# Kernel tuning notes

Measured on AMD Instinct MI355X. Metric: run time of the kernel, lower is better.

The kernel has to match this reference:

```python
import jax, jax.numpy as jnp
import numpy as np

S, L, V, E, H, LBL, CH = 4096, 16, 100000, 256, 512, 64, 4


def setup_inputs() -> dict:
    key = jax.random.key(0)
    ks = jax.random.split(key, 10)
    sc = lambda k, shp, fan: (jax.random.normal(k, shp, jnp.float32) / np.sqrt(fan)).astype(jnp.float32)
    return {
        "sentence": jax.random.randint(ks[0], (S,), 0, V, dtype=jnp.int32),
        "chars": jax.random.normal(ks[1], (S, L), dtype=jnp.float32),
        "char_lens": jax.random.randint(ks[2], (S,), 1, L + 1, dtype=jnp.int32),
        "emb": jax.random.normal(ks[3], (V, E), dtype=jnp.float32),
        "W_ih_c": sc(ks[4], (4 * CH, 1), 1),
        "W_hh_c": sc(ks[5], (4 * CH, CH), CH),
        "b_ih_c": jnp.zeros((4 * CH,), jnp.float32),
        "b_hh_c": jnp.zeros((4 * CH,), jnp.float32),
        "W_ih_w": sc(ks[6], (4 * H, E + CH), E + CH),
        "W_hh_w": sc(ks[7], (4 * H, H), H),
        "b_ih_w": jnp.zeros((4 * H,), jnp.float32),
        "b_hh_w": jnp.zeros((4 * H,), jnp.float32),
        "W_out": sc(ks[8], (LBL, H), H),
        "b_out": jnp.zeros((LBL,), jnp.float32),
    }


def _lstm_gates(gates, c):
    i, f, g, o = jnp.split(gates, 4, axis=-1)
    c_new = jax.nn.sigmoid(f) * c + jax.nn.sigmoid(i) * jnp.tanh(g)
    h_new = jax.nn.sigmoid(o) * jnp.tanh(c_new)
    return h_new, c_new


def reference(sentence, chars, char_lens, emb, W_ih_c, W_hh_c, b_ih_c, b_hh_c,
              W_ih_w, W_hh_w, b_ih_w, b_hh_w, W_out, b_out):
    s, l = chars.shape
    # --- char-level LSTM, batched over all words (ragged -> padded + mask) ---
    # input projection: input_size == 1, so gates_x[s, t] = chars[s, t] * W_ih_c[:, 0] + b_ih_c
    gx = chars[:, :, None] * W_ih_c[:, 0] + b_ih_c          # [S, L, 4*CH]
    gx_t = jnp.transpose(gx, (1, 0, 2))                      # [L, S, 4*CH]
    mask = (jnp.arange(l)[:, None] < char_lens[None, :])[:, :, None]  # [L, S, 1]

    def char_step(carry, inp):
        h, c = carry
        g, m = inp
        h_new, c_new = _lstm_gates(g + h @ W_hh_c.T + b_hh_c, c)
        return (jnp.where(m, h_new, h), jnp.where(m, c_new, c)), None

    ch0 = jnp.zeros((s, W_hh_c.shape[1]), chars.dtype)
    (h_char, _), _ = jax.lax.scan(char_step, (ch0, ch0), (gx_t, mask))  # h_char: [S, CH]

    # --- word-level LSTM over the sentence ---
    word_in = jnp.concatenate([emb[sentence], h_char], axis=-1)  # [S, E+CH]
    gx_w = word_in @ W_ih_w.T + b_ih_w                           # [S, 4*H]

    def word_step(carry, g):
        h, c = carry
        h_new, c_new = _lstm_gates(g + h @ W_hh_w.T + b_hh_w, c)
        return (h_new, c_new), h_new

    wh0 = jnp.zeros((W_hh_w.shape[1],), chars.dtype)
    _, hs = jax.lax.scan(word_step, (wh0, wh0), gx_w)            # [S, H]

    logits = hs @ W_out.T + b_out                                # [S, LBL]
    return jax.nn.log_softmax(logits, axis=-1)
```

## Files before the change

### kernel.cpp

```cpp
#include <hip/hip_runtime.h>
#include <stdint.h>

#define SLEN 4096
#define CLEN 16
#define EDIM 256
#define HDIM 512
#define CHD  4
#define NLBL 64
#define KIN  260
#define G4H  2048

typedef unsigned long long u64;

__device__ __forceinline__ float sigf(float x){ return 1.0f/(1.0f+__expf(-x)); }
__device__ __forceinline__ float ftanh(float x){
  float e = __expf(2.0f*x);
  return 1.0f - 2.0f/(e+1.0f);
}

__global__ void k_char_lstm(const float* __restrict__ chars, const int* __restrict__ lens,
                            const float* __restrict__ Wih, const float* __restrict__ Whh,
                            const float* __restrict__ bih, const float* __restrict__ bhh,
                            float* __restrict__ h_char){
  int s = blockIdx.x*blockDim.x + threadIdx.x;
  if (s >= SLEN) return;
  float wih[16], bb[16], whh[16][4];
  #pragma unroll
  for(int r=0;r<16;r++){
    wih[r]=Wih[r]; bb[r]=bih[r]+bhh[r];
    #pragma unroll
    for(int k=0;k<4;k++) whh[r][k]=Whh[r*4+k];
  }
  float x[16];
  #pragma unroll
  for(int i=0;i<4;i++){
    float4 v = *(const float4*)&chars[s*CLEN + 4*i];
    x[4*i+0]=v.x; x[4*i+1]=v.y; x[4*i+2]=v.z; x[4*i+3]=v.w;
  }
  float h[4]={0,0,0,0}, c[4]={0,0,0,0};
  int len = lens[s];
  #pragma unroll 1
  for(int t=0;t<CLEN;t++){
    float g[16];
    #pragma unroll
    for(int r=0;r<16;r++){
      float a = fmaf(x[t], wih[r], bb[r]);
      #pragma unroll
      for(int k=0;k<4;k++) a = fmaf(h[k], whh[r][k], a);
      g[r]=a;
    }
    bool m = t < len;
    #pragma unroll
    for(int j=0;j<4;j++){
      float ig=sigf(g[j]), fg=sigf(g[4+j]), gg=ftanh(g[8+j]), og=sigf(g[12+j]);
      float cn = fg*c[j] + ig*gg;
      float hn = og*ftanh(cn);
      if(m){ c[j]=cn; h[j]=hn; }
    }
  }
  #pragma unroll
  for(int j=0;j<4;j++) h_char[s*CHD+j]=h[j];
}

__global__ void k_gather(const int* __restrict__ sent, const float* __restrict__ emb,
                         const float* __restrict__ h_char, float* __restrict__ win){
  int s = blockIdx.x; int l = threadIdx.x;
  int row = sent[s];
  float4 v = *(const float4*)&emb[(size_t)row*EDIM + 4*l];
  *(float4*)&win[(size_t)s*KIN + 4*l] = v;
  if (l < CHD) win[(size_t)s*KIN + EDIM + l] = h_char[s*CHD + l];
}

#define BK 20
__global__ __launch_bounds__(256) void k_gemm_gx(const float* __restrict__ win,
                          const float* __restrict__ Wihw, float* __restrict__ gx){
  __shared__ float As[BK][68];
  __shared__ float Bs[BK][68];
  int s0 = blockIdx.x*64, n0 = blockIdx.y*64;
  int tid = threadIdx.x;
  int tm = tid>>4, tn = tid&15;
  float acc[4][4] = {};
  for(int k0=0;k0<KIN;k0+=BK){
    __syncthreads();
    #pragma unroll
    for(int i=0;i<5;i++){
      int e = tid + i*256;
      int m = e/BK, kk = e - m*BK;
      As[kk][m] = win[(size_t)(s0+m)*KIN + k0+kk];
      Bs[kk][m] = Wihw[(size_t)(n0+m)*KIN + k0+kk];
    }
    __syncthreads();
    #pragma unroll
    for(int kk=0;kk<BK;kk++){
      float4 a4 = *(const float4*)&As[kk][tm*4];
      float4 b4 = *(const float4*)&Bs[kk][tn*4];
      float av[4]={a4.x,a4.y,a4.z,a4.w};
      float bv[4]={b4.x,b4.y,b4.z,b4.w};
      #pragma unroll
      for(int i=0;i<4;i++)
        #pragma unroll
        for(int j=0;j<4;j++)
          acc[i][j] = fmaf(av[i], bv[j], acc[i][j]);
    }
  }
  #pragma unroll
  for(int i=0;i<4;i++){
    float4 o; o.x=acc[i][0]; o.y=acc[i][1]; o.z=acc[i][2]; o.w=acc[i][3];
    *(float4*)&gx[(size_t)(s0+tm*4+i)*G4H + n0 + tn*4] = o;
  }
}

__global__ __launch_bounds__(512) void k_word_lstm(const float* __restrict__ gx,
    const float* __restrict__ Whh, const float* __restrict__ bih, const float* __restrict__ bhh,
    u64* __restrict__ comm, float* __restrict__ hs){
  __shared__ float h_lds[2][8*68];
  __shared__ float gatebuf[64];
  const int tid  = threadIdx.x;
  const int g    = blockIdx.x;
  const int r    = tid>>3;
  const int cch  = tid&7;
  const int gate = r>>4, jl = r&15;
  const int R    = gate*HDIM + g*16 + jl;
  const int gi   = g*16 + tid;
  float4 w4[16];
  #pragma unroll
  for(int i=0;i<16;i++) w4[i] = *(const float4*)&Whh[(size_t)R*HDIM + cch*64 + 4*i];
  float cst = 0.f;
  float bsum[4], gxv[4];
  if (tid<16){
    #pragma unroll
    for(int q=0;q<4;q++){
      bsum[q] = bih[q*HDIM + gi] + bhh[q*HDIM + gi];
      gxv[q]  = gx[(size_t)0*G4H + q*HDIM + gi];
    }
  }

  #pragma unroll 1
  for(int t=0;t<SLEN;t++){
    float hv = 0.f;
    if (t>0){
      const u64* slot = &comm[(size_t)(t&1)*HDIM + tid];
      u64 v;
      do { v = __hip_atomic_load(slot, __ATOMIC_RELAXED, __HIP_MEMORY_SCOPE_AGENT); }
      while ((unsigned)(v>>32) != (unsigned)t);
      union{unsigned u; float f;} cv; cv.u = (unsigned)v; hv = cv.f;
    }
    const int par = t&1;
    h_lds[par][(tid>>6)*68 + (tid&63)] = hv;
    __syncthreads();
    float acc = 0.f;
    #pragma unroll
    for(int i=0;i<16;i++){
      float4 hh = *(const float4*)&h_lds[par][cch*68 + 4*i];
      acc = fmaf(w4[i].x, hh.x, acc);
      acc = fmaf(w4[i].y, hh.y, acc);
      acc = fmaf(w4[i].z, hh.z, acc);
      acc = fmaf(w4[i].w, hh.w, acc);
    }
    acc += __shfl_xor(acc,1);
    acc += __shfl_xor(acc,2);
    acc += __shfl_xor(acc,4);
    if (cch==0) gatebuf[r] = acc;
    __syncthreads();
    if (tid < 64){
      float gv  = gatebuf[tid];
      float a16 = __shfl_down(gv,16);
      float a32 = __shfl_down(gv,32);
      float a48 = __shfl_down(gv,48);
      if (tid<16){
        float gi_ = gv  + gxv[0] + bsum[0];
        float gf_ = a16 + gxv[1] + bsum[1];
        float gg_ = a32 + gxv[2] + bsum[2];
        float go_ = a48 + gxv[3] + bsum[3];
        float cn = sigf(gf_)*cst + sigf(gi_)*ftanh(gg_);
        float hn = sigf(go_)*ftanh(cn);
        cst = cn;
        union{float f; unsigned u;} hb; hb.f = hn;
        u64 pk = ((u64)(unsigned)(t+1)<<32) | (u64)hb.u;
        __hip_atomic_store(&comm[(size_t)((t+1)&1)*HDIM + gi], pk,
                           __ATOMIC_RELAXED, __HIP_MEMORY_SCOPE_AGENT);
        hs[(size_t)t*HDIM + gi] = hn;
        if (t+1 < SLEN){
          #pragma unroll
          for(int q=0;q<4;q++) gxv[q] = gx[(size_t)(t+1)*G4H + q*HDIM + gi];
        }
      }
    }
  }
}

__global__ __launch_bounds__(256) void k_out(const float* __restrict__ hs,
        const float* __restrict__ Wout, const float* __restrict__ bout,
        float* __restrict__ out){
  __shared__ float hsub[HDIM];
  __shared__ float lg[NLBL];
  int s = blockIdx.x, tid = threadIdx.x;
  hsub[tid]     = hs[(size_t)s*HDIM + tid];
  hsub[tid+256] = hs[(size_t)s*HDIM + tid + 256];
  __syncthreads();
  int l = tid>>2, q = tid&3;
  float a = 0.f;
  const float* wrp = &Wout[(size_t)l*HDIM + q*128];
  const float* hr = &hsub[q*128];
  #pragma unroll 8
  for(int i=0;i<128;i++) a = fmaf(hr[i], wrp[i], a);
  a += __shfl_xor(a,1);
  a += __shfl_xor(a,2);
  if (q==0) lg[l] = a + bout[l];
  __syncthreads();
  if (tid < NLBL){
    float x = lg[tid];
    float mx = x;
    #pragma unroll
    for(int m=32;m>=1;m>>=1) mx = fmaxf(mx, __shfl_xor(mx,m));
    float ex = __expf(x-mx);
    float sm = ex;
    #pragma unroll
    for(int m=32;m>=1;m>>=1) sm += __shfl_xor(sm,m);
    out[(size_t)s*NLBL + tid] = x - mx - __logf(sm);
  }
}

extern "C" void kernel_launch(void* const* d_in, const int* in_sizes, int n_in,
                              void* d_out, int out_size, void* d_ws, size_t ws_size,
                              hipStream_t stream){
  const int*   sent  = (const int*)d_in[0];
  const float* chars = (const float*)d_in[1];
  const int*   lens  = (const int*)d_in[2];
  const float* emb   = (const float*)d_in[3];
  const float* Wihc  = (const float*)d_in[4];
  const float* Whhc  = (const float*)d_in[5];
  const float* bihc  = (const float*)d_in[6];
  const float* bhhc  = (const float*)d_in[7];
  const float* Wihw  = (const float*)d_in[8];
  const float* Whhw  = (const float*)d_in[9];
  const float* bihw  = (const float*)d_in[10];
  const float* bhhw  = (const float*)d_in[11];
  const float* Wout  = (const float*)d_in[12];
  const float* bout  = (const float*)d_in[13];
  float* out = (float*)d_out;

  float* h_char = (float*)d_ws;
  float* win    = h_char + 16384;
  float* gx     = win + (size_t)SLEN*KIN;
  float* hs     = gx + (size_t)SLEN*G4H;
  u64*   comm   = (u64*)(hs + (size_t)SLEN*HDIM);

  k_char_lstm<<<SLEN/256, 256, 0, stream>>>(chars,lens,Wihc,Whhc,bihc,bhhc,h_char);
  k_gather<<<SLEN, 64, 0, stream>>>(sent,emb,h_char,win);
  k_gemm_gx<<<dim3(SLEN/64, G4H/64), 256, 0, stream>>>(win,Wihw,gx);
  k_word_lstm<<<HDIM/16, 512, 0, stream>>>(gx,Whhw,bihw,bhhw,comm,hs);
  k_out<<<SLEN, 256, 0, stream>>>(hs,Wout,bout,out);
}
```

Before: 6.490 ms.

## Broadcast h via readlane per wave and drop one barrier in word LSTM

Each wave now owns a 64-wide slice of the hidden vector and computes partial dot products for all 64 gate rows. The h values come from the wave's own polled lanes through readlane broadcasts, so h no longer has to be staged in LDS. Partial sums go through a double-buffered LDS array, and the extra barrier-plus-shuffle reduction is gone. Each recurrent step therefore needs one __syncthreads instead of two. In exchange, 64 scalar readlanes per step add SALU/VALU interlock cost, and the first wave does a serial 8-way sum.

```diff
diff --git a/kernel.cpp b/kernel.cpp
--- a/kernel.cpp
+++ b/kernel.cpp
@@ -17,6 +17,7 @@
   float e = __expf(2.0f*x);
   return 1.0f - 2.0f/(e+1.0f);
 }
+#define RLANE(x,i) __uint_as_float(__builtin_amdgcn_readlane(__float_as_uint(x),(i)))
 
 __global__ void k_char_lstm(const float* __restrict__ chars, const int* __restrict__ lens,
                             const float* __restrict__ Wih, const float* __restrict__ Whh,
@@ -113,18 +114,16 @@
 __global__ __launch_bounds__(512) void k_word_lstm(const float* __restrict__ gx,
     const float* __restrict__ Whh, const float* __restrict__ bih, const float* __restrict__ bhh,
     u64* __restrict__ comm, float* __restrict__ hs){
-  __shared__ float h_lds[2][8*68];
-  __shared__ float gatebuf[64];
-  const int tid  = threadIdx.x;
-  const int g    = blockIdx.x;
-  const int r    = tid>>3;
-  const int cch  = tid&7;
-  const int gate = r>>4, jl = r&15;
-  const int R    = gate*HDIM + g*16 + jl;
-  const int gi   = g*16 + tid;
+  __shared__ float pbuf[2][8][64];
+  const int tid = threadIdx.x;
+  const int g   = blockIdx.x;
+  const int w   = tid>>6;
+  const int l   = tid&63;
+  const int R   = (l>>4)*HDIM + g*16 + (l&15);
+  const int gi  = g*16 + tid;
   float4 w4[16];
   #pragma unroll
-  for(int i=0;i<16;i++) w4[i] = *(const float4*)&Whh[(size_t)R*HDIM + cch*64 + 4*i];
+  for(int i=0;i<16;i++) w4[i] = *(const float4*)&Whh[(size_t)R*HDIM + w*64 + 4*i];
   float cst = 0.f;
   float bsum[4], gxv[4];
   if (tid<16){
@@ -137,38 +136,36 @@
 
   #pragma unroll 1
   for(int t=0;t<SLEN;t++){
+    const int par = t&1;
     float hv = 0.f;
     if (t>0){
-      const u64* slot = &comm[(size_t)(t&1)*HDIM + tid];
+      const u64* slot = &comm[(size_t)par*HDIM + w*64 + l];
       u64 v;
       do { v = __hip_atomic_load(slot, __ATOMIC_RELAXED, __HIP_MEMORY_SCOPE_AGENT); }
       while ((unsigned)(v>>32) != (unsigned)t);
       union{unsigned u; float f;} cv; cv.u = (unsigned)v; hv = cv.f;
     }
-    const int par = t&1;
-    h_lds[par][(tid>>6)*68 + (tid&63)] = hv;
-    __syncthreads();
-    float acc = 0.f;
+    float a0=0.f, a1=0.f, a2=0.f, a3=0.f;
     #pragma unroll
     for(int i=0;i<16;i++){
-      float4 hh = *(const float4*)&h_lds[par][cch*68 + 4*i];
-      acc = fmaf(w4[i].x, hh.x, acc);
-      acc = fmaf(w4[i].y, hh.y, acc);
-      acc = fmaf(w4[i].z, hh.z, acc);
-      acc = fmaf(w4[i].w, hh.w, acc);
-    }
-    acc += __shfl_xor(acc,1);
-    acc += __shfl_xor(acc,2);
-    acc += __shfl_xor(acc,4);
-    if (cch==0) gatebuf[r] = acc;
+      float4 wv = w4[i];
+      a0 = fmaf(wv.x, RLANE(hv,4*i+0), a0);
+      a1 = fmaf(wv.y, RLANE(hv,4*i+1), a1);
+      a2 = fmaf(wv.z, RLANE(hv,4*i+2), a2);
+      a3 = fmaf(wv.w, RLANE(hv,4*i+3), a3);
+    }
+    pbuf[par][w][l] = (a0+a1)+(a2+a3);
     __syncthreads();
     if (tid < 64){
-      float gv  = gatebuf[tid];
-      float a16 = __shfl_down(gv,16);
-      float a32 = __shfl_down(gv,32);
-      float a48 = __shfl_down(gv,48);
+      const float* pb = &pbuf[par][0][0];
+      float s = pb[tid];
+      #pragma unroll
+      for(int q=1;q<8;q++) s += pb[q*64 + tid];
+      float a16 = __shfl_down(s,16);
+      float a32 = __shfl_down(s,32);
+      float a48 = __shfl_down(s,48);
       if (tid<16){
-        float gi_ = gv  + gxv[0] + bsum[0];
+        float gi_ = s   + gxv[0] + bsum[0];
         float gf_ = a16 + gxv[1] + bsum[1];
         float gg_ = a32 + gxv[2] + bsum[2];
         float go_ = a48 + gxv[3] + bsum[3];
```

Result: faster. 6.105 ms (-5.9%).
